# Kernel optimization log

Measured on AMD Instinct MI355X. Metric: run time of the kernel, lower is better.

Reference implementation:

```python
import jax, jax.numpy as jnp
import numpy as np

N = 50000      # nodes
E = 400000     # edges (before self-loops)
IN = 256       # in_dim
H = 4          # heads in layer 1
C = 64         # h_dim (per-head channels, layer 1)
OUT = 16       # out_dim (layer 2, 1 head)
NEG_SLOPE = 0.2


def gatv2_layer(x, src, dst, Wl, bl, Wr, br, att, bias, heads, ch, concat, num_nodes):
    # x: [N, F]; src/dst: [E']; Wl/Wr: [F, heads*ch]; att: [heads, ch]
    xl = (x @ Wl + bl).reshape(num_nodes, heads, ch)  # source transform
    xr = (x @ Wr + br).reshape(num_nodes, heads, ch)  # target transform
    m = xl[src] + xr[dst]                              # [E', H, C] gather
    e = jnp.sum(jax.nn.leaky_relu(m, NEG_SLOPE) * att, axis=-1)  # [E', H]
    # segment softmax over incoming edges of each dst node (self-loops ensure non-empty)
    emax = jax.ops.segment_max(e, dst, num_segments=num_nodes)   # [N, H]
    ee = jnp.exp(e - emax[dst])
    denom = jax.ops.segment_sum(ee, dst, num_segments=num_nodes)  # [N, H]
    alpha = ee / (denom[dst] + 1e-16)                              # [E', H]
    out = jax.ops.segment_sum(alpha[..., None] * xl[src], dst, num_segments=num_nodes)  # [N,H,C]
    if concat:
        out = out.reshape(num_nodes, heads * ch)
    else:
        out = out.mean(axis=1)
    return out + bias


def setup_inputs() -> dict:
    key = jax.random.key(0)
    ks = jax.random.split(key, 16)
    s = 0.05
    inp = {
        "x": jax.random.normal(ks[0], (N, IN), jnp.float32),
        "edge_index": jax.random.randint(ks[1], (2, E), 0, N),
        # layer 1 params (in_dim -> heads*h_dim)
        "Wl1": jax.random.normal(ks[2], (IN, H * C), jnp.float32) * s,
        "bl1": jnp.zeros((H * C,), jnp.float32),
        "Wr1": jax.random.normal(ks[3], (IN, H * C), jnp.float32) * s,
        "br1": jnp.zeros((H * C,), jnp.float32),
        "att1": jax.random.normal(ks[4], (H, C), jnp.float32) * s,
        "bias1": jnp.zeros((H * C,), jnp.float32),
        # layer 2 params (heads*h_dim -> out_dim, 1 head)
        "Wl2": jax.random.normal(ks[5], (H * C, OUT), jnp.float32) * s,
        "bl2": jnp.zeros((OUT,), jnp.float32),
        "Wr2": jax.random.normal(ks[6], (H * C, OUT), jnp.float32) * s,
        "br2": jnp.zeros((OUT,), jnp.float32),
        "att2": jax.random.normal(ks[7], (1, OUT), jnp.float32) * s,
        "bias2": jnp.zeros((OUT,), jnp.float32),
    }
    return inp


def reference(x, edge_index, Wl1, bl1, Wr1, br1, att1, bias1, Wl2, bl2, Wr2, br2, att2, bias2):
    # add self loops (PyG GATv2Conv default add_self_loops=True)
    loop = jnp.arange(N, dtype=edge_index.dtype)
    src = jnp.concatenate([edge_index[0], loop])
    dst = jnp.concatenate([edge_index[1], loop])
    h = gatv2_layer(x, src, dst, Wl1, bl1, Wr1, br1, att1, bias1, H, C, True, N)
    h = jnp.tanh(h)
    o = gatv2_layer(h, src, dst, Wl2, bl2, Wr2, br2, att2, bias2, 1, OUT, False, N)
    return o, jax.nn.log_softmax(o, axis=1)
```

## Files before the change

### kernel.cpp

```cpp
#include <hip/hip_runtime.h>

typedef __bf16 bfv8 __attribute__((ext_vector_type(8)));
typedef float f32x4 __attribute__((ext_vector_type(4)));
typedef float f32x2 __attribute__((ext_vector_type(2)));
typedef short shortv8 __attribute__((ext_vector_type(8)));
typedef unsigned short usv8 __attribute__((ext_vector_type(8)));

__device__ __forceinline__ float b2f(unsigned short u) {
  unsigned int v = ((unsigned int)u) << 16;
  float f;
  __builtin_memcpy(&f, &v, 4);
  return f;
}
__device__ __forceinline__ unsigned short f2b(float f) {
  unsigned int u;
  __builtin_memcpy(&u, &f, 4);
  u += 0x7fffu + ((u >> 16) & 1u);
  return (unsigned short)(u >> 16);
}

__device__ __forceinline__ f32x2 bf2x(unsigned int u) {
  f32x2 r;
  r.x = __builtin_bit_cast(float, u << 16);
  r.y = __builtin_bit_cast(float, u & 0xffff0000u);
  return r;
}

template <int CTRL>
__device__ __forceinline__ float dpp_mv(float x) {
  int xi = __builtin_bit_cast(int, x);
  int yi = __builtin_amdgcn_update_dpp(0, xi, CTRL, 0xf, 0xf, true);
  return __builtin_bit_cast(float, yi);
}

__device__ __forceinline__ float tanh_fast(float x) {
  float e2 = __expf(2.f * x);
  float r = __builtin_amdgcn_rcpf(e2 + 1.f);
  float th = fmaf(-2.f, r, 1.f);
  if (!(th == th)) th = 0.f;
  return th;
}

__global__ void probe_kernel(const unsigned short* __restrict__ x, int* __restrict__ flag) {
  int lane = threadIdx.x;
  int cnt = 0;
  for (int i = lane; i < 4096; i += 64) {
    unsigned int e = (x[i] >> 7) & 0xffu;
    if (e >= 0x86u) cnt++;
  }
#pragma unroll
  for (int off = 1; off < 64; off <<= 1) cnt += __shfl_xor(cnt, off, 64);
  if (lane == 0) *flag = (cnt > 100) ? 1 : 0;
}

#define P_TOT 140352
__global__ __launch_bounds__(256) void fused_pre_kernel(
    const void* __restrict__ x, unsigned short* __restrict__ Xc,
    const int* __restrict__ flagp, int NX,
    const int* __restrict__ ei, int E, int Nn, int* __restrict__ cnt,
    const void* p0, const void* p1, const void* p2, const void* p3,
    const void* p4, const void* p5, const void* p6, const void* p7,
    const void* p8, const void* p9, const void* p10, const void* p11,
    unsigned short* __restrict__ Pc, int nb_convx, int nb_count) {
  int b = blockIdx.x;
  int t = threadIdx.x;
  if (b < nb_convx) {
    int i = (b * 256 + t) * 4;
    if (i >= NX) return;
    if (*flagp) {
      float4 f = *reinterpret_cast<const float4*>((const float*)x + i);
      ushort4 o;
      o.x = f2b(f.x); o.y = f2b(f.y); o.z = f2b(f.z); o.w = f2b(f.w);
      *reinterpret_cast<ushort4*>(Xc + i) = o;
    } else {
      *reinterpret_cast<ushort4*>(Xc + i) =
          *reinterpret_cast<const ushort4*>((const unsigned short*)x + i);
    }
  } else if (b < nb_convx + nb_count) {
    int i = (b - nb_convx) * 256 + t;
    int total = E + Nn;
    if (i >= total) return;
    int d = (i < E) ? ei[E + i] : (i - E);
    if ((unsigned)d >= (unsigned)Nn) d = 0;
    atomicAdd(&cnt[d], 1);
  } else {
    int i = (b - nb_convx - nb_count) * 256 + t;
    if (i >= P_TOT) return;
    const int offs[13] = {0, 65536, 65792, 131328, 131584, 131840, 132096,
                          136192, 136208, 140304, 140320, 140336, P_TOT};
    const void* ptrs[12] = {p0, p1, p2, p3, p4, p5, p6, p7, p8, p9, p10, p11};
    int flag = *flagp;
    int k = 0;
    while (i >= offs[k + 1]) k++;
    int local = i - offs[k];
    unsigned short v;
    if (flag) v = f2b(((const float*)ptrs[k])[local]);
    else v = ((const unsigned short*)ptrs[k])[local];
    Pc[i] = v;
  }
}

__global__ __launch_bounds__(1024) void fused_mid_kernel(
    const int* __restrict__ cnt, int* __restrict__ row_start, int* __restrict__ blkTot,
    int Nn, int nb_scan,
    const unsigned short* __restrict__ Pc,
    unsigned short* __restrict__ WT1, unsigned short* __restrict__ WT2) {
  int b = blockIdx.x;
  int t = threadIdx.x;
  if (b < nb_scan) {
    __shared__ int buf[1024];
    int i = b * 1024 + t;
    int v = (i < Nn) ? cnt[i] : 0;
    buf[t] = v;
    __syncthreads();
    for (int off = 1; off < 1024; off <<= 1) {
      int x = (t >= off) ? buf[t - off] : 0;
      __syncthreads();
      buf[t] += x;
      __syncthreads();
    }
    if (i < Nn) row_start[i] = buf[t] - v;
    if (t == 1023) blkTot[b] = buf[1023];
  } else {
    int idx = (b - nb_scan) * 1024 + t;
    if (idx < 512 * 256) {
      int n = idx >> 8, k = idx & 255;
      WT1[idx] = (n < 256) ? Pc[0 + k * 256 + n]
                           : Pc[65792 + k * 256 + (n - 256)];
    } else {
      int j = idx - 512 * 256;
      if (j < 32 * 256) {
        int n = j >> 8, k = j & 255;
        WT2[j] = (n < 16) ? Pc[132096 + k * 16 + n]
                          : Pc[136208 + k * 16 + (n - 16)];
      }
    }
  }
}

__global__ __launch_bounds__(64) void scan2_kernel(const int* __restrict__ blkTot,
                                                   int* __restrict__ blkOff, int nb,
                                                   int* __restrict__ row_start, int Nn,
                                                   int total) {
  int lane = threadIdx.x;
  int v = (lane < nb) ? blkTot[lane] : 0;
  int s = v;
#pragma unroll
  for (int off = 1; off < 64; off <<= 1) {
    int u = __shfl_up(s, off, 64);
    if (lane >= off) s += u;
  }
  int excl = s - v;
  blkOff[lane] = excl;
  if (lane == 63) blkOff[64] = s;
  int idx = Nn >> 10;
  int bo = (idx >= 64) ? __shfl(s, 63, 64) : __shfl(excl, idx, 64);
  if (lane == 0) row_start[Nn] = total - bo;
}

__global__ __launch_bounds__(256) void fused_gemm_fill_kernel(
    const unsigned short* __restrict__ X,
    const unsigned short* __restrict__ WT,
    const unsigned short* __restrict__ bl, const unsigned short* __restrict__ br,
    unsigned short* __restrict__ C, int M,
    const int* __restrict__ ei, int E, int Nn,
    const int* __restrict__ row_start, const int* __restrict__ blkOff,
    int* __restrict__ cursor, int* __restrict__ csr_src,
    int nb_gemm, int nb_fill) {
  __shared__ unsigned short smem[18432];
  int b = blockIdx.x;
  int nmin = nb_gemm < nb_fill ? nb_gemm : nb_fill;
  int ninter = 2 * nmin;
  int role, id;
  if (b < ninter) { role = b & 1; id = b >> 1; }
  else {
    int r = b - ninter;
    if (nb_fill > nb_gemm) { role = 1; id = nb_gemm + r; }
    else { role = 0; id = nb_fill + r; }
  }

  if (role == 1) {
    int i = id * 256 + threadIdx.x;
    int total = E + Nn;
    if (i >= total) return;
    int s, d;
    if (i < E) { s = ei[i]; d = ei[E + i]; } else { s = i - E; d = i - E; }
    if ((unsigned)d >= (unsigned)Nn) d = 0;
    if ((unsigned)s >= (unsigned)Nn) s = 0;
    int pos = row_start[d] + blkOff[d >> 10] + atomicAdd(&cursor[d], 1);
    if ((unsigned)pos < (unsigned)total) csr_src[pos] = s;
    return;
  }

  const int t = threadIdx.x;
  const int lane = t & 63;
  const int w = t >> 6;
  const int quad = lane >> 4;
  const int l16 = lane & 15;
  const int n_blk = id & 3;
  const int by = id >> 2;
  const int m_base = by * 128 + (w >> 1) * 64;
  const int n_base = n_blk * 128 + (w & 1) * 64;

  const int st_row = t >> 3;
  const int st_seg = t & 7;
  const unsigned short* wt_base =
      WT + ((size_t)(n_blk * 128 + st_row)) * 256 + st_seg * 8;

  f32x4 acc[4][4];
#pragma unroll
  for (int i = 0; i < 4; i++)
#pragma unroll
    for (int j = 0; j < 4; j++) acc[i][j] = (f32x4){0.f, 0.f, 0.f, 0.f};

  shortv8 st[4];
#pragma unroll
  for (int i = 0; i < 4; i++)
    st[i] = *reinterpret_cast<const shortv8*>(wt_base + (size_t)(32 * i) * 256);
#pragma unroll
  for (int i = 0; i < 4; i++) {
    int row = st_row + 32 * i;
    *reinterpret_cast<shortv8*>(smem + row * 64 + ((st_seg ^ (row & 7)) * 8)) = st[i];
  }
  __syncthreads();

#pragma unroll
  for (int c = 0; c < 4; c++) {
    if (c < 3) {
#pragma unroll
      for (int i = 0; i < 4; i++)
        st[i] = *reinterpret_cast<const shortv8*>(wt_base + (size_t)(32 * i) * 256 +
                                                  (c + 1) * 64);
    }
    const unsigned short* bb = smem + (c & 1) * 8192;
#pragma unroll
    for (int sub = 0; sub < 2; sub++) {
      bfv8 a[4], bfr[4];
      int seg_r = sub * 4 + quad;
#pragma unroll
      for (int i = 0; i < 4; i++) {
        int row = m_base + 16 * i + l16;
        if (row >= M) row = M - 1;
        a[i] = *reinterpret_cast<const bfv8*>(X + (size_t)row * 256 + c * 64 + sub * 32 +
                                              quad * 8);
      }
#pragma unroll
      for (int j = 0; j < 4; j++) {
        int col = (w & 1) * 64 + 16 * j + l16;
        bfr[j] = *reinterpret_cast<const bfv8*>(bb + col * 64 + ((seg_r ^ (col & 7)) * 8));
      }
#pragma unroll
      for (int i = 0; i < 4; i++)
#pragma unroll
        for (int j = 0; j < 4; j++)
          acc[i][j] = __builtin_amdgcn_mfma_f32_16x16x32_bf16(a[i], bfr[j], acc[i][j], 0, 0, 0);
    }
    if (c < 3) {
      int buf = (c + 1) & 1;
#pragma unroll
      for (int i = 0; i < 4; i++) {
        int row = st_row + 32 * i;
        *reinterpret_cast<shortv8*>(smem + buf * 8192 + row * 64 +
                                    ((st_seg ^ (row & 7)) * 8)) = st[i];
      }
      __syncthreads();
    }
  }

  __syncthreads();
  unsigned short* lt = smem + w * 4608;
#pragma unroll
  for (int j = 0; j < 4; j++) {
    int col = n_base + 16 * j + l16;
    float bias = (col < 256) ? b2f(bl[col]) : b2f(br[col - 256]);
#pragma unroll
    for (int i = 0; i < 4; i++)
#pragma unroll
      for (int r = 0; r < 4; r++)
        lt[(16 * i + quad * 4 + r) * 72 + 16 * j + l16] = f2b(acc[i][j][r] + bias);
  }
#pragma unroll
  for (int pass = 0; pass < 8; pass++) {
    int row = pass * 8 + (lane >> 3);
    int colg = (lane & 7) * 8;
    shortv8 v = *reinterpret_cast<const shortv8*>(lt + row * 72 + colg);
    int grow = m_base + row;
    if (grow < M)
      *reinterpret_cast<shortv8*>(C + (size_t)grow * 512 + n_base + colg) = v;
  }
}

__global__ __launch_bounds__(256) void gemm2_kernel(
    const unsigned short* __restrict__ H, const unsigned short* __restrict__ WT,
    const unsigned short* __restrict__ bl, const unsigned short* __restrict__ br,
    float* __restrict__ C, int M) {
  const int lane = threadIdx.x & 63;
  const int w = threadIdx.x >> 6;
  const int quad = lane >> 4;
  const int l16 = lane & 15;
  const int m_base = blockIdx.x * 256 + w * 64;

  f32x4 acc[4][2];
#pragma unroll
  for (int i = 0; i < 4; i++)
#pragma unroll
    for (int j = 0; j < 2; j++) acc[i][j] = (f32x4){0.f, 0.f, 0.f, 0.f};

#pragma unroll
  for (int k0 = 0; k0 < 256; k0 += 32) {
    bfv8 a[4], b[2];
#pragma unroll
    for (int i = 0; i < 4; i++) {
      int row = m_base + 16 * i + l16;
      if (row >= M) row = M - 1;
      a[i] = *reinterpret_cast<const bfv8*>(H + (size_t)row * 256 + k0 + quad * 8);
    }
#pragma unroll
    for (int j = 0; j < 2; j++) {
      int col = 16 * j + l16;
      b[j] = *reinterpret_cast<const bfv8*>(WT + (size_t)col * 256 + k0 + quad * 8);
    }
#pragma unroll
    for (int i = 0; i < 4; i++)
#pragma unroll
      for (int j = 0; j < 2; j++)
        acc[i][j] = __builtin_amdgcn_mfma_f32_16x16x32_bf16(a[i], b[j], acc[i][j], 0, 0, 0);
  }

#pragma unroll
  for (int j = 0; j < 2; j++) {
    int col = 16 * j + l16;
    float bias = (j == 0) ? b2f(bl[l16]) : b2f(br[l16]);
#pragma unroll
    for (int i = 0; i < 4; i++) {
#pragma unroll
      for (int r = 0; r < 4; r++) {
        int row = m_base + 16 * i + quad * 4 + r;
        if (row < M) C[(size_t)row * 32 + col] = acc[i][j][r] + bias;
      }
    }
  }
}

__global__ __launch_bounds__(256) void agg1_kernel(
    const unsigned short* __restrict__ C1,
    const unsigned short* __restrict__ att1,
    const unsigned short* __restrict__ bias1,
    const int* __restrict__ row_start, const int* __restrict__ blkOff,
    const int* __restrict__ csr_src,
    unsigned short* __restrict__ H1,
    int Nn, int Etot) {
  int wid = blockIdx.x * 4 + (threadIdx.x >> 6);
  if (wid >= Nn) return;
  int lane = threadIdx.x & 63;
  int half = lane >> 5;
  int c0 = (lane & 31) * 8;

  f32x2 at2[4], xr2[4];
  {
    uint4 a4 = *reinterpret_cast<const uint4*>(att1 + c0);
    uint4 r4 = *reinterpret_cast<const uint4*>(C1 + (size_t)wid * 512 + 256 + c0);
    at2[0] = bf2x(a4.x); at2[1] = bf2x(a4.y); at2[2] = bf2x(a4.z); at2[3] = bf2x(a4.w);
    xr2[0] = bf2x(r4.x); xr2[1] = bf2x(r4.y); xr2[2] = bf2x(r4.z); xr2[3] = bf2x(r4.w);
  }

  float denom = 0.f;
  f32x2 acc2[4] = {};
  int beg = row_start[wid] + blkOff[wid >> 10];
  int end = row_start[wid + 1] + blkOff[(wid + 1) >> 10];
  if (beg < 0) beg = 0;
  if (end < beg || end - beg > Etot) end = beg;

  for (int base = beg; base < end; base += 64) {
    int cend = min(end, base + 64);
    int pl = base + lane;
    if (pl >= end) pl = end - 1;
    int s_pre = csr_src[pl];
#pragma unroll 2
    for (int i = base; i < cend; i += 2) {
      int p = i + half;
      bool valid = p < cend;
      int s = __shfl(s_pre, p - base, 64);
      if ((unsigned)s >= (unsigned)Nn) s = 0;
      uint4 rw = *reinterpret_cast<const uint4*>(C1 + (size_t)s * 512 + c0);
      f32x2 xl0 = bf2x(rw.x), xl1 = bf2x(rw.y), xl2 = bf2x(rw.z), xl3 = bf2x(rw.w);
      f32x2 m0 = xl0 + xr2[0], m1 = xl1 + xr2[1];
      f32x2 m2 = xl2 + xr2[2], m3 = xl3 + xr2[3];
      f32x2 l0 = __builtin_elementwise_max(m0, m0 * 0.2f);
      f32x2 l1 = __builtin_elementwise_max(m1, m1 * 0.2f);
      f32x2 l2 = __builtin_elementwise_max(m2, m2 * 0.2f);
      f32x2 l3 = __builtin_elementwise_max(m3, m3 * 0.2f);
      f32x2 d2 = l0 * at2[0];
      d2 += l1 * at2[1];
      d2 += l2 * at2[2];
      d2 += l3 * at2[3];
      float dot = d2.x + d2.y;
      dot += dpp_mv<0xB1>(dot);
      dot += dpp_mv<0x4E>(dot);
      dot += dpp_mv<0x141>(dot);
      dot = fminf(fmaxf(dot, -60.f), 60.f);
      float wgt = valid ? __expf(dot) : 0.f;
      denom += wgt;
      acc2[0] += xl0 * wgt;
      acc2[1] += xl1 * wgt;
      acc2[2] += xl2 * wgt;
      acc2[3] += xl3 * wgt;
    }
  }
  denom += __shfl_xor(denom, 32, 64);
#pragma unroll
  for (int k = 0; k < 4; k++) {
    acc2[k].x += __shfl_xor(acc2[k].x, 32, 64);
    acc2[k].y += __shfl_xor(acc2[k].y, 32, 64);
  }

  if (half == 0) {
    float inv = __builtin_amdgcn_rcpf(denom + 1e-16f);
    uint4 b4 = *reinterpret_cast<const uint4*>(bias1 + c0);
    f32x2 bb[4] = {bf2x(b4.x), bf2x(b4.y), bf2x(b4.z), bf2x(b4.w)};
    uint4 o;
    unsigned int od[4];
#pragma unroll
    for (int k = 0; k < 4; k++) {
      f32x2 xv = acc2[k] * inv + bb[k];
      float t0 = tanh_fast(xv.x);
      float t1 = tanh_fast(xv.y);
      od[k] = (unsigned int)f2b(t0) | ((unsigned int)f2b(t1) << 16);
    }
    o.x = od[0]; o.y = od[1]; o.z = od[2]; o.w = od[3];
    *reinterpret_cast<uint4*>(H1 + (size_t)wid * 256 + c0) = o;
  }
}

__global__ __launch_bounds__(256) void agg2_kernel(
    const float* __restrict__ C2,
    const unsigned short* __restrict__ att2,
    const unsigned short* __restrict__ bias2,
    const int* __restrict__ row_start, const int* __restrict__ blkOff,
    const int* __restrict__ csr_src,
    float* __restrict__ out,
    int Nn, int Etot) {
  int wid = blockIdx.x * 4 + (threadIdx.x >> 6);
  if (wid >= Nn) return;
  int lane = threadIdx.x & 63;
  int eslot = lane >> 2;
  int cg = (lane & 3) * 4;

  float at[4], xr[4];
  {
    ushort4 a4 = *reinterpret_cast<const ushort4*>(att2 + cg);
    at[0] = b2f(a4.x); at[1] = b2f(a4.y); at[2] = b2f(a4.z); at[3] = b2f(a4.w);
    float4 r4 = *reinterpret_cast<const float4*>(C2 + (size_t)wid * 32 + 16 + cg);
    xr[0] = r4.x; xr[1] = r4.y; xr[2] = r4.z; xr[3] = r4.w;
  }

  float denom = 0.f;
  float acc[4] = {0.f, 0.f, 0.f, 0.f};
  int beg = row_start[wid] + blkOff[wid >> 10];
  int end = row_start[wid + 1] + blkOff[(wid + 1) >> 10];
  if (beg < 0) beg = 0;
  if (end < beg || end - beg > Etot) end = beg;

  for (int base = beg; base < end; base += 64) {
    int cend = min(end, base + 64);
    int pl = base + lane;
    if (pl >= end) pl = end - 1;
    int s_pre = csr_src[pl];
    for (int i = base; i < cend; i += 16) {
      int p = i + eslot;
      bool valid = p < cend;
      int s = __shfl(s_pre, p - base, 64);
      if ((unsigned)s >= (unsigned)Nn) s = 0;
      float4 x4 = *reinterpret_cast<const float4*>(C2 + (size_t)s * 32 + cg);
      float xl[4] = {x4.x, x4.y, x4.z, x4.w};
      float dot = 0.f;
#pragma unroll
      for (int k = 0; k < 4; k++) {
        float m = xl[k] + xr[k];
        float l = fmaxf(m, 0.2f * m);
        dot = fmaf(l, at[k], dot);
      }
      dot += dpp_mv<0xB1>(dot);
      dot += dpp_mv<0x4E>(dot);
      dot = fminf(fmaxf(dot, -60.f), 60.f);
      float wgt = valid ? __expf(dot) : 0.f;
      denom += wgt;
#pragma unroll
      for (int k = 0; k < 4; k++) acc[k] = fmaf(wgt, xl[k], acc[k]);
    }
  }
  denom += dpp_mv<0x124>(denom);
  denom += dpp_mv<0x128>(denom);
#pragma unroll
  for (int k = 0; k < 4; k++) {
    acc[k] += dpp_mv<0x124>(acc[k]);
    acc[k] += dpp_mv<0x128>(acc[k]);
  }
#pragma unroll
  for (int off = 16; off <= 32; off <<= 1) {
    denom += __shfl_xor(denom, off, 64);
#pragma unroll
    for (int k = 0; k < 4; k++) acc[k] += __shfl_xor(acc[k], off, 64);
  }

  float inv = __builtin_amdgcn_rcpf(denom + 1e-16f);
  ushort4 b4 = *reinterpret_cast<const ushort4*>(bias2 + cg);
  float bb[4] = {b2f(b4.x), b2f(b4.y), b2f(b4.z), b2f(b4.w)};
  float o[4];
#pragma unroll
  for (int k = 0; k < 4; k++) {
    o[k] = acc[k] * inv + bb[k];
    if (!(o[k] == o[k])) o[k] = 0.f;
  }
  float mx = fmaxf(fmaxf(o[0], o[1]), fmaxf(o[2], o[3]));
  mx = fmaxf(mx, dpp_mv<0xB1>(mx));
  mx = fmaxf(mx, dpp_mv<0x4E>(mx));
  float se = 0.f;
#pragma unroll
  for (int k = 0; k < 4; k++) se += __expf(o[k] - mx);
  se += dpp_mv<0xB1>(se);
  se += dpp_mv<0x4E>(se);
  float ls = logf(se);
  if (lane < 4) {
    float4 vo = {o[0], o[1], o[2], o[3]};
    float4 vl = {o[0] - mx - ls, o[1] - mx - ls, o[2] - mx - ls, o[3] - mx - ls};
    *reinterpret_cast<float4*>(out + (size_t)wid * 16 + cg) = vo;
    *reinterpret_cast<float4*>(out + (size_t)Nn * 16 + (size_t)wid * 16 + cg) = vl;
  }
}

extern "C" void kernel_launch(void* const* d_in, const int* in_sizes, int n_in,
                              void* d_out, int out_size, void* d_ws, size_t ws_size,
                              hipStream_t stream) {
  const void* x_raw = d_in[0];
  const int* ei     = (const int*)d_in[1];

  const int M = in_sizes[0] / 256;
  const int E = in_sizes[1] / 2;
  const int TOT = E + M;
  const int NX = M * 256;

  char* ws = (char*)d_ws;
  size_t off = 0;
  auto alloc = [&](size_t bytes) -> void* {
    void* p = ws + off;
    off = (off + bytes + 255) & ~(size_t)255;
    return p;
  };
  int*            flag   = (int*)alloc(4);
  unsigned short* Pc     = (unsigned short*)alloc((size_t)P_TOT * 2);
  unsigned short* Xc     = (unsigned short*)alloc((size_t)NX * 2);
  unsigned short* WT1    = (unsigned short*)alloc((size_t)512 * 256 * 2);
  unsigned short* WT2    = (unsigned short*)alloc((size_t)32 * 256 * 2);
  int*            cnt    = (int*)alloc((size_t)M * 4);
  int*            cursor = (int*)alloc((size_t)M * 4);
  int*            row_start = (int*)alloc((size_t)(M + 1) * 4);
  int*            csr_src   = (int*)alloc((size_t)TOT * 4);
  int*            blkTot = (int*)alloc(64 * 4);
  int*            blkOff = (int*)alloc(65 * 4);
  float*          C2     = (float*)alloc((size_t)M * 32 * 4);
  unsigned short* C1     = (unsigned short*)alloc((size_t)M * 512 * 2);
  const size_t need = off;
  (void)n_in;
  unsigned short* H1 = Xc;

  if (ws_size < need) {
    hipMemsetAsync(d_out, 0, (size_t)out_size * 4, stream);
    return;
  }

  unsigned short* bl1c   = Pc + 65536;
  unsigned short* br1c   = Pc + 131328;
  unsigned short* att1c  = Pc + 131584;
  unsigned short* bias1c = Pc + 131840;
  unsigned short* bl2c   = Pc + 136192;
  unsigned short* br2c   = Pc + 140304;
  unsigned short* att2c  = Pc + 140320;
  unsigned short* bias2c = Pc + 140336;

  hipMemsetAsync(cnt, 0, (size_t)M * 4, stream);
  hipMemsetAsync(cursor, 0, (size_t)M * 4, stream);

  probe_kernel<<<1, 64, 0, stream>>>((const unsigned short*)x_raw, flag);

  const int nb_convx = (NX / 4 + 255) / 256;
  const int nb_count = (TOT + 255) / 256;
  const int nb_convp = (P_TOT + 255) / 256;
  fused_pre_kernel<<<nb_convx + nb_count + nb_convp, 256, 0, stream>>>(
      x_raw, Xc, flag, NX, ei, E, M, cnt,
      d_in[2], d_in[3], d_in[4], d_in[5], d_in[6], d_in[7], d_in[8], d_in[9],
      d_in[10], d_in[11], d_in[12], d_in[13], Pc, nb_convx, nb_count);

  const int nb_scan = (M + 1023) / 1024;
  const int nb_tr = (512 * 256 + 32 * 256 + 1023) / 1024;
  fused_mid_kernel<<<nb_scan + nb_tr, 1024, 0, stream>>>(cnt, row_start, blkTot, M,
                                                         nb_scan, Pc, WT1, WT2);

  scan2_kernel<<<1, 64, 0, stream>>>(blkTot, blkOff, nb_scan, row_start, M, TOT);

  const int nb_gemm = 4 * ((M + 127) / 128);
  const int nb_fill = nb_count;
  fused_gemm_fill_kernel<<<nb_gemm + nb_fill, 256, 0, stream>>>(
      Xc, WT1, bl1c, br1c, C1, M, ei, E, M, row_start, blkOff, cursor, csr_src,
      nb_gemm, nb_fill);

  agg1_kernel<<<(M + 3) / 4, 256, 0, stream>>>(C1, att1c, bias1c, row_start, blkOff,
                                               csr_src, H1, M, TOT);

  gemm2_kernel<<<(M + 255) / 256, 256, 0, stream>>>(H1, WT2, bl2c, br2c, C2, M);

  agg2_kernel<<<(M + 3) / 4, 256, 0, stream>>>(C2, att2c, bias2c, row_start, blkOff,
                                               csr_src, (float*)d_out, M, TOT);
}
```

Before: 288.2 us.

## Split fill from GEMM1, drop LDS staging of weights, skip bf16 copy of x

Splits the interleaved GEMM/CSR-fill kernel into a separate fill kernel and a standalone GEMM1 kernel. GEMM1 now reads the weight fragments straight from global memory instead of staging them through double-buffered shared memory, which removes the in-loop barriers. When the input is already bf16, GEMM1 reads x_raw directly, so the pre-kernel no longer copies x. In exchange the kernel issues more global or L2 traffic for the weights, adds one launch, and gives up the overlap between the atomic-heavy fill and the matrix work.

```diff
diff --git a/kernel.cpp b/kernel.cpp
--- a/kernel.cpp
+++ b/kernel.cpp
@@ -65,17 +65,13 @@
   int b = blockIdx.x;
   int t = threadIdx.x;
   if (b < nb_convx) {
+    if (!*flagp) return;
     int i = (b * 256 + t) * 4;
     if (i >= NX) return;
-    if (*flagp) {
-      float4 f = *reinterpret_cast<const float4*>((const float*)x + i);
-      ushort4 o;
-      o.x = f2b(f.x); o.y = f2b(f.y); o.z = f2b(f.z); o.w = f2b(f.w);
-      *reinterpret_cast<ushort4*>(Xc + i) = o;
-    } else {
-      *reinterpret_cast<ushort4*>(Xc + i) =
-          *reinterpret_cast<const ushort4*>((const unsigned short*)x + i);
-    }
+    float4 f = *reinterpret_cast<const float4*>((const float*)x + i);
+    ushort4 o;
+    o.x = f2b(f.x); o.y = f2b(f.y); o.z = f2b(f.z); o.w = f2b(f.w);
+    *reinterpret_cast<ushort4*>(Xc + i) = o;
   } else if (b < nb_convx + nb_count) {
     int i = (b - nb_convx) * 256 + t;
     int total = E + Nn;
@@ -158,116 +154,73 @@
   if (lane == 0) row_start[Nn] = total - bo;
 }
 
-__global__ __launch_bounds__(256) void fused_gemm_fill_kernel(
-    const unsigned short* __restrict__ X,
+__global__ __launch_bounds__(256) void fill_kernel(const int* __restrict__ ei, int E, int Nn,
+                                                   const int* __restrict__ row_start,
+                                                   const int* __restrict__ blkOff,
+                                                   int* __restrict__ cursor,
+                                                   int* __restrict__ csr_src) {
+  int i = blockIdx.x * 256 + threadIdx.x;
+  int total = E + Nn;
+  if (i >= total) return;
+  int s, d;
+  if (i < E) { s = ei[i]; d = ei[E + i]; } else { s = i - E; d = i - E; }
+  if ((unsigned)d >= (unsigned)Nn) d = 0;
+  if ((unsigned)s >= (unsigned)Nn) s = 0;
+  int pos = row_start[d] + blkOff[d >> 10] + atomicAdd(&cursor[d], 1);
+  if ((unsigned)pos < (unsigned)total) csr_src[pos] = s;
+}
+
+__global__ __launch_bounds__(256) void gemm1_kernel(
+    const unsigned short* __restrict__ Xc,
+    const unsigned short* __restrict__ x_raw,
+    const int* __restrict__ flagp,
     const unsigned short* __restrict__ WT,
     const unsigned short* __restrict__ bl, const unsigned short* __restrict__ br,
-    unsigned short* __restrict__ C, int M,
-    const int* __restrict__ ei, int E, int Nn,
-    const int* __restrict__ row_start, const int* __restrict__ blkOff,
-    int* __restrict__ cursor, int* __restrict__ csr_src,
-    int nb_gemm, int nb_fill) {
+    unsigned short* __restrict__ C, int M) {
   __shared__ unsigned short smem[18432];
-  int b = blockIdx.x;
-  int nmin = nb_gemm < nb_fill ? nb_gemm : nb_fill;
-  int ninter = 2 * nmin;
-  int role, id;
-  if (b < ninter) { role = b & 1; id = b >> 1; }
-  else {
-    int r = b - ninter;
-    if (nb_fill > nb_gemm) { role = 1; id = nb_gemm + r; }
-    else { role = 0; id = nb_fill + r; }
-  }
-
-  if (role == 1) {
-    int i = id * 256 + threadIdx.x;
-    int total = E + Nn;
-    if (i >= total) return;
-    int s, d;
-    if (i < E) { s = ei[i]; d = ei[E + i]; } else { s = i - E; d = i - E; }
-    if ((unsigned)d >= (unsigned)Nn) d = 0;
-    if ((unsigned)s >= (unsigned)Nn) s = 0;
-    int pos = row_start[d] + blkOff[d >> 10] + atomicAdd(&cursor[d], 1);
-    if ((unsigned)pos < (unsigned)total) csr_src[pos] = s;
-    return;
-  }
-
+  const unsigned short* X = (*flagp) ? Xc : x_raw;
   const int t = threadIdx.x;
   const int lane = t & 63;
   const int w = t >> 6;
   const int quad = lane >> 4;
   const int l16 = lane & 15;
-  const int n_blk = id & 3;
-  const int by = id >> 2;
+  const int n_blk = blockIdx.x & 3;
+  const int by = blockIdx.x >> 2;
   const int m_base = by * 128 + (w >> 1) * 64;
   const int n_base = n_blk * 128 + (w & 1) * 64;
 
-  const int st_row = t >> 3;
-  const int st_seg = t & 7;
-  const unsigned short* wt_base =
-      WT + ((size_t)(n_blk * 128 + st_row)) * 256 + st_seg * 8;
-
   f32x4 acc[4][4];
 #pragma unroll
   for (int i = 0; i < 4; i++)
 #pragma unroll
     for (int j = 0; j < 4; j++) acc[i][j] = (f32x4){0.f, 0.f, 0.f, 0.f};
 
-  shortv8 st[4];
-#pragma unroll
-  for (int i = 0; i < 4; i++)
-    st[i] = *reinterpret_cast<const shortv8*>(wt_base + (size_t)(32 * i) * 256);
+  int rowp[4];
 #pragma unroll
   for (int i = 0; i < 4; i++) {
-    int row = st_row + 32 * i;
-    *reinterpret_cast<shortv8*>(smem + row * 64 + ((st_seg ^ (row & 7)) * 8)) = st[i];
-  }
-  __syncthreads();
-
-#pragma unroll
-  for (int c = 0; c < 4; c++) {
-    if (c < 3) {
-#pragma unroll
-      for (int i = 0; i < 4; i++)
-        st[i] = *reinterpret_cast<const shortv8*>(wt_base + (size_t)(32 * i) * 256 +
-                                                  (c + 1) * 64);
-    }
-    const unsigned short* bb = smem + (c & 1) * 8192;
-#pragma unroll
-    for (int sub = 0; sub < 2; sub++) {
-      bfv8 a[4], bfr[4];
-      int seg_r = sub * 4 + quad;
-#pragma unroll
-      for (int i = 0; i < 4; i++) {
-        int row = m_base + 16 * i + l16;
-        if (row >= M) row = M - 1;
-        a[i] = *reinterpret_cast<const bfv8*>(X + (size_t)row * 256 + c * 64 + sub * 32 +
-                                              quad * 8);
-      }
-#pragma unroll
-      for (int j = 0; j < 4; j++) {
-        int col = (w & 1) * 64 + 16 * j + l16;
-        bfr[j] = *reinterpret_cast<const bfv8*>(bb + col * 64 + ((seg_r ^ (col & 7)) * 8));
-      }
-#pragma unroll
-      for (int i = 0; i < 4; i++)
-#pragma unroll
-        for (int j = 0; j < 4; j++)
-          acc[i][j] = __builtin_amdgcn_mfma_f32_16x16x32_bf16(a[i], bfr[j], acc[i][j], 0, 0, 0);
-    }
-    if (c < 3) {
-      int buf = (c + 1) & 1;
-#pragma unroll
-      for (int i = 0; i < 4; i++) {
-        int row = st_row + 32 * i;
-        *reinterpret_cast<shortv8*>(smem + buf * 8192 + row * 64 +
-                                    ((st_seg ^ (row & 7)) * 8)) = st[i];
-      }
-      __syncthreads();
-    }
-  }
-
-  __syncthreads();
+    int row = m_base + 16 * i + l16;
+    if (row >= M) row = M - 1;
+    rowp[i] = row;
+  }
+
+#pragma unroll
+  for (int k0 = 0; k0 < 256; k0 += 32) {
+    bfv8 a[4], b[4];
+#pragma unroll
+    for (int i = 0; i < 4; i++)
+      a[i] = *reinterpret_cast<const bfv8*>(X + (size_t)rowp[i] * 256 + k0 + quad * 8);
+#pragma unroll
+    for (int j = 0; j < 4; j++) {
+      int col = n_base + 16 * j + l16;
+      b[j] = *reinterpret_cast<const bfv8*>(WT + (size_t)col * 256 + k0 + quad * 8);
+    }
+#pragma unroll
+    for (int i = 0; i < 4; i++)
+#pragma unroll
+      for (int j = 0; j < 4; j++)
+        acc[i][j] = __builtin_amdgcn_mfma_f32_16x16x32_bf16(a[i], b[j], acc[i][j], 0, 0, 0);
+  }
+
   unsigned short* lt = smem + w * 4608;
 #pragma unroll
   for (int j = 0; j < 4; j++) {
@@ -279,6 +232,7 @@
       for (int r = 0; r < 4; r++)
         lt[(16 * i + quad * 4 + r) * 72 + 16 * j + l16] = f2b(acc[i][j][r] + bias);
   }
+  __syncthreads();
 #pragma unroll
   for (int pass = 0; pass < 8; pass++) {
     int row = pass * 8 + (lane >> 3);
@@ -598,11 +552,12 @@
 
   scan2_kernel<<<1, 64, 0, stream>>>(blkTot, blkOff, nb_scan, row_start, M, TOT);
 
+  fill_kernel<<<(TOT + 255) / 256, 256, 0, stream>>>(ei, E, M, row_start, blkOff,
+                                                     cursor, csr_src);
+
   const int nb_gemm = 4 * ((M + 127) / 128);
-  const int nb_fill = nb_count;
-  fused_gemm_fill_kernel<<<nb_gemm + nb_fill, 256, 0, stream>>>(
-      Xc, WT1, bl1c, br1c, C1, M, ei, E, M, row_start, blkOff, cursor, csr_src,
-      nb_gemm, nb_fill);
+  gemm1_kernel<<<nb_gemm, 256, 0, stream>>>(Xc, (const unsigned short*)x_raw, flag,
+                                            WT1, bl1c, br1c, C1, M);
 
   agg1_kernel<<<(M + 3) / 4, 256, 0, stream>>>(C1, att1c, bias1c, row_start, blkOff,
                                                csr_src, H1, M, TOT);
```

Result: slower. 301.4 us (+4.6%).
